# Optimization experiments

Hardware: AMD Instinct MI355X
Metric: run time of the kernel (lower is better)

## Reference

```python
import jax, jax.numpy as jnp
import numpy as np

NUM_CAMS = 4
E = 256          # embed_dim
H_HEADS = 8      # num_heads
DH = E // H_HEADS
CIN = 64
FF = 4 * E
N_LAYERS = 2
EPS = 1e-5


def _layer_norm(x, g, b):
    mu = jnp.mean(x, axis=-1, keepdims=True)
    var = jnp.mean((x - mu) ** 2, axis=-1, keepdims=True)
    return (x - mu) * jax.lax.rsqrt(var + EPS) * g + b


def setup_inputs() -> dict:
    key = jax.random.key(0)
    ks = jax.random.split(key, 20)
    s = 0.02
    inp = {
        "features": jax.random.normal(ks[0], (NUM_CAMS, 2, CIN, 96, 96), jnp.float32),
        # 1x1 input projection conv
        "Wp": jax.random.normal(ks[1], (E, CIN), jnp.float32) * s,
        "bp": jnp.zeros((E,), jnp.float32),
        # per-layer attention params (stacked over 2 layers)
        "Wqkv": jax.random.normal(ks[2], (N_LAYERS, 3 * E, E), jnp.float32) * s,
        "bqkv": jnp.zeros((N_LAYERS, 3 * E), jnp.float32),
        "Wo": jax.random.normal(ks[3], (N_LAYERS, E, E), jnp.float32) * s,
        "bo": jnp.zeros((N_LAYERS, E), jnp.float32),
        # FFN
        "W1": jax.random.normal(ks[4], (N_LAYERS, FF, E), jnp.float32) * s,
        "b1": jnp.zeros((N_LAYERS, FF), jnp.float32),
        "W2": jax.random.normal(ks[5], (N_LAYERS, E, FF), jnp.float32) * s,
        "b2": jnp.zeros((N_LAYERS, E), jnp.float32),
        # LayerNorms
        "g1": jnp.ones((N_LAYERS, E), jnp.float32),
        "be1": jnp.zeros((N_LAYERS, E), jnp.float32),
        "g2": jnp.ones((N_LAYERS, E), jnp.float32),
        "be2": jnp.zeros((N_LAYERS, E), jnp.float32),
        # 1x1 output conv
        "Wout": jax.random.normal(ks[6], (CIN, E), jnp.float32) * s,
        "bout": jnp.zeros((CIN,), jnp.float32),
    }
    return inp


def reference(features, Wp, bp, Wqkv, bqkv, Wo, bo, W1, b1, W2, b2,
              g1, be1, g2, be2, Wout, bout):
    n_cam, B, Cin, Hh, Ww = features.shape
    # 1x1 conv projection + rearrange to per-pixel sequences: [B*H*W, n_cam, E]
    x = jnp.einsum('nbchw,ec->bhwne', features, Wp) + bp
    x = x.reshape(B * Hh * Ww, n_cam, E)

    scale = 1.0 / jnp.sqrt(jnp.float32(DH))
    for i in range(N_LAYERS):
        # self-attention (post-norm encoder layer, dropout=identity in eval)
        qkv = x @ Wqkv[i].T + bqkv[i]                      # [N, S, 3E]
        q, k, v = jnp.split(qkv, 3, axis=-1)
        q = q.reshape(-1, n_cam, H_HEADS, DH)
        k = k.reshape(-1, n_cam, H_HEADS, DH)
        v = v.reshape(-1, n_cam, H_HEADS, DH)
        scores = jnp.einsum('nqhd,nkhd->nhqk', q, k) * scale
        attn = jax.nn.softmax(scores, axis=-1)
        sa = jnp.einsum('nhqk,nkhd->nqhd', attn, v).reshape(-1, n_cam, E)
        sa = sa @ Wo[i].T + bo[i]
        x = _layer_norm(x + sa, g1[i], be1[i])
        # FFN (ReLU activation, default)
        ff = jax.nn.relu(x @ W1[i].T + b1[i]) @ W2[i].T + b2[i]
        x = _layer_norm(x + ff, g2[i], be2[i])

    # mean over cameras, back to [B, C, H, W] via 1x1 output conv
    fused = x.mean(axis=1).reshape(B, Hh, Ww, E)
    out = jnp.einsum('bhwe,ce->bchw', fused, Wout) + bout[None, :, None, None]
    return out
```

## Files before the change

kernel.cpp:

```cpp
#include <hip/hip_runtime.h>
#include <cstdint>
#include <cstddef>


typedef __bf16 bf16;
typedef __bf16 bf16x8 __attribute__((ext_vector_type(8)));
typedef __bf16 bf16x4 __attribute__((ext_vector_type(4)));
typedef float  f32x4  __attribute__((ext_vector_type(4)));

__device__ __forceinline__ void async_copy16(const void* g, void* l)
{
    __builtin_amdgcn_global_load_lds(
        (__attribute__((address_space(1))) void*)g,
        (__attribute__((address_space(3))) void*)l,
        16, 0, 0);
}

__global__ void pack_all_k(const float* __restrict__ s0, const float* __restrict__ s1,
                           const float* __restrict__ s2, const float* __restrict__ s3,
                           const float* __restrict__ s4,
                           bf16* __restrict__ d0, bf16* __restrict__ d1,
                           bf16* __restrict__ d2, bf16* __restrict__ d3,
                           bf16* __restrict__ d4)
{
    const int i = blockIdx.x * 256 + threadIdx.x;
    if (i < 393216)       d0[i] = (bf16)s0[i];
    else if (i < 524288)  d1[i - 393216] = (bf16)s1[i - 393216];
    else if (i < 1048576) d2[i - 524288] = (bf16)s2[i - 524288];
    else if (i < 1572864) d3[i - 1048576] = (bf16)s3[i - 1048576];
    else                  d4[i - 1572864] = (bf16)s4[i - 1572864];
}

__global__ void pack_w2f_k(const float* __restrict__ W2, bf16* __restrict__ W2F)
{
    const int g  = blockIdx.x * 256 + threadIdx.x;
    const int l  = g >> 15;
    const int e  = g & 32767;
    const int nt   = e >> 11;
    const int rem  = e & 2047;
    const int kc   = rem >> 6;
    const int lane = rem & 63;
    const int row  = nt * 16 + (lane & 15);
    const int col  = kc * 32 + (lane >> 4) * 8;
    const float* src = W2 + (size_t)l * 262144;
    bf16x8 v;
#pragma unroll
    for (int q = 0; q < 8; ++q) v[q] = (bf16)src[(size_t)row * 1024 + col + q];
    *(bf16x8*)(W2F + (size_t)l * 262144 + (size_t)e * 8) = v;
}

__global__ __launch_bounds__(256) void feat_pack_k(const float* __restrict__ feat,
                                                   bf16* __restrict__ Xf)
{
    __shared__ float ft[64][68];

    const int tid  = threadIdx.x;
    const int camb = blockIdx.y;
    const int cam  = camb >> 1;
    const int b    = camb & 1;
    const int hw0  = blockIdx.x * 64;

    const float* fb = feat + (size_t)camb * 64 * 9216 + hw0;
#pragma unroll
    for (int rep = 0; rep < 16; ++rep) {
        const int idx = rep * 256 + tid;
        const int c = idx >> 6, p = idx & 63;
        ft[p][c] = fb[(size_t)c * 9216 + p];
    }
    __syncthreads();

    const int pbase = b * 9216 + hw0;
#pragma unroll
    for (int rep = 0; rep < 2; ++rep) {
        const int idx = rep * 256 + tid;
        const int p = idx >> 3, cc = idx & 7;
        const f32x4 a = *(const f32x4*)(&ft[p][cc * 8]);
        const f32x4 c4 = *(const f32x4*)(&ft[p][cc * 8 + 4]);
        bf16x8 v;
#pragma unroll
        for (int i = 0; i < 4; ++i) { v[i] = (bf16)a[i]; v[4 + i] = (bf16)c4[i]; }
        const size_t t = (size_t)(pbase + p) * 4 + cam;
        *(bf16x8*)(Xf + t * 64 + cc * 8) = v;
    }
}

template <bool RELU>
__global__ __launch_bounds__(256, 2) void gemm_bt(
    const bf16* __restrict__ A, const bf16* __restrict__ B,
    const float* __restrict__ bias, bf16* __restrict__ C,
    int N, int K)
{
    __shared__ __align__(16) bf16 As[128 * 64];
    __shared__ __align__(16) bf16 Bs[128 * 64];

    const int tid  = threadIdx.x;
    const int lane = tid & 63;
    const int wv   = tid >> 6;
    const int wm   = wv >> 1;
    const int wn   = wv & 1;
    const int bm   = blockIdx.y * 128;
    const int bn   = blockIdx.x * 128;

    const int r8  = lane >> 3;
    const int p8  = lane & 7;
    const int gch = p8 ^ r8;

    const int quad = lane >> 4;
    const int l16  = lane & 15;

    f32x4 acc[4][4] = {};

    for (int k0 = 0; k0 < K; k0 += 64) {
#pragma unroll
        for (int inst = 0; inst < 4; ++inst) {
            const int row = wv * 32 + inst * 8 + r8;
            const bf16* ga = A + (size_t)(bm + row) * K + (k0 + gch * 8);
            const bf16* gb = B + (size_t)(bn + row) * K + (k0 + gch * 8);
            async_copy16(ga, (char*)As + (wv * 4 + inst) * 1024);
            async_copy16(gb, (char*)Bs + (wv * 4 + inst) * 1024);
        }
        __syncthreads();

#pragma unroll
        for (int kk = 0; kk < 2; ++kk) {
            bf16x8 af[4], bfr[4];
            const int lch = kk * 4 + quad;
#pragma unroll
            for (int i = 0; i < 4; ++i) {
                const int m = wm * 64 + i * 16 + l16;
                af[i] = *(const bf16x8*)((const char*)As + (m * 8 + (lch ^ (m & 7))) * 16);
                const int n = wn * 64 + i * 16 + l16;
                bfr[i] = *(const bf16x8*)((const char*)Bs + (n * 8 + (lch ^ (n & 7))) * 16);
            }
#pragma unroll
            for (int i = 0; i < 4; ++i)
#pragma unroll
                for (int j = 0; j < 4; ++j)
                    acc[i][j] = __builtin_amdgcn_mfma_f32_16x16x32_bf16(
                        af[i], bfr[j], acc[i][j], 0, 0, 0);
        }
        __syncthreads();
    }

#pragma unroll
    for (int j = 0; j < 4; ++j) {
        const int n = bn + wn * 64 + j * 16 + l16;
        const float bv = bias[n];
#pragma unroll
        for (int i = 0; i < 4; ++i) {
            const int mb = bm + wm * 64 + i * 16 + quad * 4;
#pragma unroll
            for (int r = 0; r < 4; ++r) {
                float v = acc[i][j][r] + bv;
                if (RELU) v = fmaxf(v, 0.f);
                C[(size_t)(mb + r) * N + n] = (bf16)v;
            }
        }
    }
}

__global__ __launch_bounds__(256, 2) void gemm_ln_k(
    const bf16* __restrict__ A, const bf16* __restrict__ B,
    const float* __restrict__ bias, const bf16* __restrict__ Xres,
    const float* __restrict__ gam, const float* __restrict__ bet,
    bf16* __restrict__ Xout, int K)
{
    __shared__ __align__(16) bf16 S[24576];
    __shared__ float2 red[128][2];

    const int tid  = threadIdx.x;
    const int lane = tid & 63;
    const int wv   = tid >> 6;
    const int wm   = wv >> 1;
    const int wn   = wv & 1;
    const int bm   = blockIdx.x * 128;
    const int quad = lane >> 4;
    const int l16  = lane & 15;

    f32x4 acc[4][8] = {};

    for (int k0 = 0; k0 < K; k0 += 64) {
#pragma unroll
        for (int s = 0; s < 12; ++s) {
            const int L   = s * 256 + tid;
            const int row = L >> 3;
            const int gch = (L & 7) ^ (row & 7);
            const bf16* g = (row < 128)
                ? A + (size_t)(bm + row) * K + (k0 + gch * 8)
                : B + (size_t)(row - 128) * K + (k0 + gch * 8);
            async_copy16(g, (char*)S + (size_t)L * 16);
        }
        __syncthreads();

#pragma unroll
        for (int kk = 0; kk < 2; ++kk) {
            const int lch = kk * 4 + quad;
            bf16x8 af[4], bfr[8];
#pragma unroll
            for (int i = 0; i < 4; ++i) {
                const int m = wm * 64 + i * 16 + l16;
                af[i] = *(const bf16x8*)((const char*)S + (m * 8 + (lch ^ (m & 7))) * 16);
            }
#pragma unroll
            for (int j = 0; j < 8; ++j) {
                const int n = wn * 128 + j * 16 + l16;
                bfr[j] = *(const bf16x8*)((const char*)S + ((128 + n) * 8 + (lch ^ (n & 7))) * 16);
            }
#pragma unroll
            for (int i = 0; i < 4; ++i)
#pragma unroll
                for (int j = 0; j < 8; ++j)
                    acc[i][j] = __builtin_amdgcn_mfma_f32_16x16x32_bf16(
                        af[i], bfr[j], acc[i][j], 0, 0, 0);
        }
        __syncthreads();
    }

    float bv[8], gv[8], bev[8];
#pragma unroll
    for (int j = 0; j < 8; ++j) {
        const int n = wn * 128 + j * 16 + l16;
        bv[j] = bias[n]; gv[j] = gam[n]; bev[j] = bet[n];
    }

#pragma unroll
    for (int i = 0; i < 4; ++i) {
#pragma unroll
        for (int r = 0; r < 4; ++r) {
            const int rl  = wm * 64 + i * 16 + quad * 4 + r;
            const size_t row = (size_t)(bm + rl);
            float s1 = 0.f, s2 = 0.f;
#pragma unroll
            for (int j = 0; j < 8; ++j) {
                const int n = wn * 128 + j * 16 + l16;
                const float v = acc[i][j][r] + bv[j] + (float)Xres[row * 256 + n];
                acc[i][j][r] = v;
                s1 += v; s2 += v * v;
            }
#pragma unroll
            for (int off = 1; off < 16; off <<= 1) {
                s1 += __shfl_xor(s1, off, 64);
                s2 += __shfl_xor(s2, off, 64);
            }
            if (l16 == 0) red[rl][wn] = make_float2(s1, s2);
        }
    }
    __syncthreads();

#pragma unroll
    for (int i = 0; i < 4; ++i) {
#pragma unroll
        for (int r = 0; r < 4; ++r) {
            const int rl = wm * 64 + i * 16 + quad * 4 + r;
            const float2 p0 = red[rl][0], p1 = red[rl][1];
            const float mu  = (p0.x + p1.x) * (1.f / 256.f);
            const float ex2 = (p0.y + p1.y) * (1.f / 256.f);
            const float rstd = rsqrtf(fmaxf(ex2 - mu * mu, 0.f) + 1e-5f);
            const size_t row = (size_t)(bm + rl);
#pragma unroll
            for (int j = 0; j < 8; ++j) {
                const int n = wn * 128 + j * 16 + l16;
                Xout[row * 256 + n] = (bf16)((acc[i][j][r] - mu) * rstd * gv[j] + bev[j]);
            }
        }
    }
}

__device__ __forceinline__ void ffn_stage_w1(int st, const bf16* __restrict__ W1,
                                             char* stg, int tid)
{
    char* buf = stg + (size_t)(st & 1) * 16384;
    const int hc = st >> 2;
    const int q  = st & 3;
#pragma unroll
    for (int it = 0; it < 4; ++it) {
        const int L = it * 256 + tid;
        const int row = L >> 3, psl = L & 7;
        const int c = psl ^ (row & 7);
        async_copy16(W1 + (size_t)(hc * 128 + row) * 256 + q * 64 + c * 8,
                     buf + (size_t)L * 16);
    }
}

__global__ __launch_bounds__(256, 2) void ffn_fused_k(
    const bf16* __restrict__ X,
    const bf16* __restrict__ W1, const float* __restrict__ b1,
    const bf16* __restrict__ W2f, const float* __restrict__ b2,
    const float* __restrict__ gam, const float* __restrict__ bet,
    bf16* __restrict__ Xout)
{
    __shared__ __align__(16) char smem[81920];
    bf16* Xs = (bf16*)smem;
    bf16* Ts = (bf16*)(smem + 32768);
    float2 (*red)[2] = (float2 (*)[2])(void*)(smem + 32768);
    char* stg = smem + 49152;

    const int tid  = threadIdx.x;
    const int lane = tid & 63;
    const int wv   = tid >> 6;
    const int wm   = wv >> 1;
    const int wn   = wv & 1;
    const int quad = lane >> 4;
    const int l16  = lane & 15;
    const int bm   = blockIdx.x * 64;

#pragma unroll
    for (int it = 0; it < 8; ++it) {
        const int L = it * 256 + tid;
        const int row = L >> 5, slot = L & 31;
        const int gch = (slot & 24) | ((slot ^ row) & 7);
        async_copy16(X + (size_t)(bm + row) * 256 + gch * 8,
                     (char*)Xs + (size_t)L * 16);
    }
    ffn_stage_w1(0, W1, stg, tid);
    __syncthreads();

    f32x4 acc2[2][8] = {};

#pragma unroll 1
    for (int hc = 0; hc < 8; ++hc) {
        f32x4 accA[2][4] = {};

#pragma unroll
        for (int q = 0; q < 4; ++q) {
            const int st = hc * 4 + q;
            if (st + 1 < 32) ffn_stage_w1(st + 1, W1, stg, tid);
            const char* cur = stg + (size_t)(st & 1) * 16384;
#pragma unroll
            for (int kk = 0; kk < 2; ++kk) {
                const int ch = kk * 4 + quad;
                const int gc = q * 8 + ch;
                bf16x8 af[2], bfr[4];
#pragma unroll
                for (int i = 0; i < 2; ++i) {
                    const int m  = wm * 32 + i * 16 + l16;
                    const int sl = (gc & 24) | ((gc ^ m) & 7);
                    af[i] = *(const bf16x8*)((const char*)Xs + (m * 32 + sl) * 16);
                }
#pragma unroll
                for (int j = 0; j < 4; ++j) {
                    const int n  = wn * 64 + j * 16 + l16;
                    const int sl = ch ^ (n & 7);
                    bfr[j] = *(const bf16x8*)(cur + (n * 8 + sl) * 16);
                }
#pragma unroll
                for (int i = 0; i < 2; ++i)
#pragma unroll
                    for (int j = 0; j < 4; ++j)
                        accA[i][j] = __builtin_amdgcn_mfma_f32_16x16x32_bf16(
                            af[i], bfr[j], accA[i][j], 0, 0, 0);
            }
            if (q == 3) {
#pragma unroll
                for (int j = 0; j < 4; ++j) {
                    const int h  = wn * 64 + j * 16 + l16;
                    const float bb = b1[hc * 128 + h];
                    const int g  = h >> 3;
#pragma unroll
                    for (int i = 0; i < 2; ++i)
#pragma unroll
                        for (int r = 0; r < 4; ++r) {
                            const int m  = wm * 32 + i * 16 + quad * 4 + r;
                            const int sl = (g & 8) | ((g ^ m) & 7);
                            const float v = fmaxf(accA[i][j][r] + bb, 0.f);
                            *((bf16*)((char*)Ts + (m * 16 + sl) * 16 + (h & 7) * 2)) = (bf16)v;
                        }
                }
            }
            __syncthreads();
        }

#pragma unroll 2
        for (int kc = 0; kc < 4; ++kc) {
            const int tc = kc * 4 + quad;
            bf16x8 af[2], bfr[8];
#pragma unroll
            for (int i = 0; i < 2; ++i) {
                const int m  = wm * 32 + i * 16 + l16;
                const int sl = (tc & 8) | ((tc ^ m) & 7);
                af[i] = *(const bf16x8*)((const char*)Ts + (m * 16 + sl) * 16);
            }
            const int kcg = hc * 4 + kc;
#pragma unroll
            for (int j = 0; j < 8; ++j) {
                const int nt = wn * 8 + j;
                bfr[j] = *(const bf16x8*)(W2f + ((size_t)(nt * 32 + kcg) * 64 + lane) * 8);
            }
#pragma unroll
            for (int i = 0; i < 2; ++i)
#pragma unroll
                for (int j = 0; j < 8; ++j)
                    acc2[i][j] = __builtin_amdgcn_mfma_f32_16x16x32_bf16(
                        af[i], bfr[j], acc2[i][j], 0, 0, 0);
        }
    }

    __syncthreads();

    float bv[8], gv[8], bev[8];
#pragma unroll
    for (int j = 0; j < 8; ++j) {
        const int n = wn * 128 + j * 16 + l16;
        bv[j] = b2[n]; gv[j] = gam[n]; bev[j] = bet[n];
    }

#pragma unroll
    for (int i = 0; i < 2; ++i) {
#pragma unroll
        for (int r = 0; r < 4; ++r) {
            const int rl = wm * 32 + i * 16 + quad * 4 + r;
            float s1 = 0.f, s2 = 0.f;
#pragma unroll
            for (int j = 0; j < 8; ++j) {
                const int n  = wn * 128 + j * 16 + l16;
                const int gc = n >> 3;
                const int sl = (gc & 24) | ((gc ^ rl) & 7);
                const float xr = (float)*((const bf16*)((const char*)Xs +
                                   (rl * 32 + sl) * 16 + (n & 7) * 2));
                const float v = acc2[i][j][r] + bv[j] + xr;
                acc2[i][j][r] = v;
                s1 += v; s2 += v * v;
            }
#pragma unroll
            for (int off = 1; off < 16; off <<= 1) {
                s1 += __shfl_xor(s1, off, 64);
                s2 += __shfl_xor(s2, off, 64);
            }
            if (l16 == 0) red[rl][wn] = make_float2(s1, s2);
        }
    }
    __syncthreads();

#pragma unroll
    for (int i = 0; i < 2; ++i) {
#pragma unroll
        for (int r = 0; r < 4; ++r) {
            const int rl = wm * 32 + i * 16 + quad * 4 + r;
            const float2 p0 = red[rl][0], p1 = red[rl][1];
            const float mu  = (p0.x + p1.x) * (1.f / 256.f);
            const float ex2 = (p0.y + p1.y) * (1.f / 256.f);
            const float rstd = rsqrtf(fmaxf(ex2 - mu * mu, 0.f) + 1e-5f);
            const size_t row = (size_t)(bm + rl);
#pragma unroll
            for (int j = 0; j < 8; ++j) {
                const int n = wn * 128 + j * 16 + l16;
                Xout[row * 256 + n] = (bf16)((acc2[i][j][r] - mu) * rstd * gv[j] + bev[j]);
            }
        }
    }
}

__global__ __launch_bounds__(256) void attention_k(const bf16* __restrict__ QKV,
                                                   bf16* __restrict__ SA)
{
    __shared__ float qf[4][4][768];
    __shared__ float sc[4][8][4][4];

    const int tid  = threadIdx.x;
    const int wv   = tid >> 6;
    const int lane = tid & 63;
    const int s    = blockIdx.x * 4 + wv;

    const bf16* base = QKV + (size_t)s * 4 * 768;
#pragma unroll
    for (int it = 0; it < 6; ++it) {
        const int idx = it * 64 + lane;
        const bf16x8 v = *(const bf16x8*)(base + idx * 8);
        const int tok = idx / 96;
        const int e   = (idx % 96) * 8;
        f32x4 f0, f1;
#pragma unroll
        for (int i = 0; i < 4; ++i) { f0[i] = (float)v[i]; f1[i] = (float)v[4 + i]; }
        *(f32x4*)(&qf[wv][tok][e])     = f0;
        *(f32x4*)(&qf[wv][tok][e + 4]) = f1;
    }
    __syncthreads();

#pragma unroll
    for (int rep = 0; rep < 2; ++rep) {
        const int t = rep * 64 + lane;
        const int h = t >> 4, i = (t >> 2) & 3, j = t & 3;
        const float* q = &qf[wv][i][h * 32];
        const float* k = &qf[wv][j][256 + h * 32];
        float a = 0.f;
#pragma unroll
        for (int dd = 0; dd < 32; ++dd) {
            const int d = (dd + lane) & 31;
            a += q[d] * k[d];
        }
        sc[wv][h][i][j] = a * 0.17677669529663687f;
    }
    __syncthreads();

    if (lane < 32) {
        const int h = lane >> 2, i = lane & 3;
        float s0 = sc[wv][h][i][0], s1 = sc[wv][h][i][1];
        float s2 = sc[wv][h][i][2], s3 = sc[wv][h][i][3];
        float m = fmaxf(fmaxf(s0, s1), fmaxf(s2, s3));
        float e0 = expf(s0 - m), e1 = expf(s1 - m);
        float e2 = expf(s2 - m), e3 = expf(s3 - m);
        float inv = 1.f / (e0 + e1 + e2 + e3);
        sc[wv][h][i][0] = e0 * inv;
        sc[wv][h][i][1] = e1 * inv;
        sc[wv][h][i][2] = e2 * inv;
        sc[wv][h][i][3] = e3 * inv;
    }
    __syncthreads();

    const int h = lane >> 3;
#pragma unroll
    for (int i = 0; i < 4; ++i) {
        f32x4 a = {0.f, 0.f, 0.f, 0.f};
#pragma unroll
        for (int j = 0; j < 4; ++j) {
            const float p = sc[wv][h][i][j];
            const f32x4 v = *(const f32x4*)(&qf[wv][j][512 + lane * 4]);
#pragma unroll
            for (int q = 0; q < 4; ++q) a[q] += p * v[q];
        }
        bf16x4 o;
#pragma unroll
        for (int q = 0; q < 4; ++q) o[q] = (bf16)a[q];
        *(bf16x4*)(SA + (size_t)(s * 4 + i) * 256 + lane * 4) = o;
    }
}

__global__ __launch_bounds__(256) void out_proj_k(const bf16* __restrict__ X,
                                                  const float* __restrict__ Wout,
                                                  const float* __restrict__ bout,
                                                  float* __restrict__ out)
{
    __shared__ float fused[16][260];
    const int tid = threadIdx.x;
    const int p0  = blockIdx.x * 16;

#pragma unroll
    for (int it = 0; it < 16; ++it) {
        const int idx = it * 256 + tid;
        const int pix = idx >> 8, e = idx & 255;
        const size_t base = (size_t)(p0 + pix) * 1024 + e;
        const float s = (float)X[base] + (float)X[base + 256] +
                        (float)X[base + 512] + (float)X[base + 768];
        fused[pix][e] = s * 0.25f;
    }
    __syncthreads();

    const int pix = tid & 15;
    const int c0  = tid >> 4;
    const int p   = p0 + pix;
    const int b   = p / 9216;
    const int hw  = p % 9216;
#pragma unroll
    for (int it = 0; it < 4; ++it) {
        const int c = it * 16 + c0;
        const float* w = Wout + c * 256;
        float acc = bout[c];
#pragma unroll 8
        for (int e = 0; e < 256; ++e) acc += fused[pix][e] * w[e];
        out[((size_t)b * 64 + c) * 9216 + hw] = acc;
    }
}

extern "C" void kernel_launch(void* const* d_in, const int* in_sizes, int n_in,
                              void* d_out, int out_size, void* d_ws, size_t ws_size,
                              hipStream_t stream)
{
    const float* features = (const float*)d_in[0];
    const float* Wp   = (const float*)d_in[1];
    const float* bp   = (const float*)d_in[2];
    const float* Wqkv = (const float*)d_in[3];
    const float* bqkv = (const float*)d_in[4];
    const float* Wo   = (const float*)d_in[5];
    const float* bo   = (const float*)d_in[6];
    const float* W1   = (const float*)d_in[7];
    const float* b1   = (const float*)d_in[8];
    const float* W2   = (const float*)d_in[9];
    const float* b2   = (const float*)d_in[10];
    const float* g1   = (const float*)d_in[11];
    const float* be1  = (const float*)d_in[12];
    const float* g2   = (const float*)d_in[13];
    const float* be2  = (const float*)d_in[14];
    const float* Wout = (const float*)d_in[15];
    const float* bout = (const float*)d_in[16];
    float* out = (float*)d_out;

    char* ws = (char*)d_ws;
    bf16* X   = (bf16*)(ws);
    bf16* QKV = (bf16*)(ws + 37748736ull);
    bf16* SAb = (bf16*)(ws + 150994944ull);
    bf16* Xf  = (bf16*)(ws + 188743680ull);
    bf16* WpB = (bf16*)(ws + 198180864ull);
    bf16* W2F = (bf16*)(ws + 198213632ull);
    bf16* Wb  = (bf16*)(ws + 226492416ull);

    bf16* WqkvB = Wb;
    bf16* WoB   = Wb + 393216;
    bf16* W1B   = Wb + 524288;

    pack_all_k<<<6208, 256, 0, stream>>>(Wqkv, Wo, W1, W2, Wp,
                                         WqkvB, WoB, W1B, Wb + 1048576, WpB);
    pack_w2f_k<<<256, 256, 0, stream>>>(W2, W2F);

    feat_pack_k<<<dim3(144, 8), 256, 0, stream>>>(features, Xf);
    gemm_bt<false><<<dim3(2, 576), 256, 0, stream>>>(Xf, WpB, bp, X, 256, 64);

    for (int l = 0; l < 2; ++l) {
        gemm_bt<false><<<dim3(6, 576), 256, 0, stream>>>(
            X, WqkvB + l * 196608, bqkv + l * 768, QKV, 768, 256);
        attention_k<<<4608, 256, 0, stream>>>(QKV, SAb);
        gemm_ln_k<<<576, 256, 0, stream>>>(
            SAb, WoB + l * 65536, bo + l * 256, X,
            g1 + l * 256, be1 + l * 256, X, 256);
        ffn_fused_k<<<1152, 256, 0, stream>>>(
            X, W1B + l * 262144, b1 + l * 1024,
            W2F + l * 262144, b2 + l * 256,
            g2 + l * 256, be2 + l * 256, X);
    }

    out_proj_k<<<1152, 256, 0, stream>>>(X, Wout, bout, out);
}
```

Baseline: 661.8 us.

## Pre-swizzle W1 and Wqkv into MFMA fragment layout, read B directly from global

Weights for the QKV projection and the FFN's first matmul are repacked once into the MFMA B-fragment order. The kernels then load B operands straight from global (L2-cached) memory instead of staging them in LDS through double buffers. A new dedicated QKV GEMM keeps the whole 128x256 A tile in LDS. This removes LDS staging traffic and most barriers in the FFN and shrinks its LDS footprint, at the cost of global-latency-bound B loads that are no longer prefetched.

```diff
diff --git a/kernel.cpp b/kernel.cpp
--- a/kernel.cpp
+++ b/kernel.cpp
@@ -16,37 +16,40 @@
         16, 0, 0);
 }
 
-__global__ void pack_all_k(const float* __restrict__ s0, const float* __restrict__ s1,
-                           const float* __restrict__ s2, const float* __restrict__ s3,
-                           const float* __restrict__ s4,
-                           bf16* __restrict__ d0, bf16* __restrict__ d1,
-                           bf16* __restrict__ d2, bf16* __restrict__ d3,
-                           bf16* __restrict__ d4)
+__global__ void pack_all_k(const float* __restrict__ Wo, const float* __restrict__ Wp,
+                           bf16* __restrict__ WoB, bf16* __restrict__ WpB)
 {
     const int i = blockIdx.x * 256 + threadIdx.x;
-    if (i < 393216)       d0[i] = (bf16)s0[i];
-    else if (i < 524288)  d1[i - 393216] = (bf16)s1[i - 393216];
-    else if (i < 1048576) d2[i - 524288] = (bf16)s2[i - 524288];
-    else if (i < 1572864) d3[i - 1048576] = (bf16)s3[i - 1048576];
-    else                  d4[i - 1572864] = (bf16)s4[i - 1572864];
-}
-
-__global__ void pack_w2f_k(const float* __restrict__ W2, bf16* __restrict__ W2F)
-{
-    const int g  = blockIdx.x * 256 + threadIdx.x;
-    const int l  = g >> 15;
-    const int e  = g & 32767;
-    const int nt   = e >> 11;
-    const int rem  = e & 2047;
+    if (i < 131072)      WoB[i] = (bf16)Wo[i];
+    else if (i < 147456) WpB[i - 131072] = (bf16)Wp[i - 131072];
+}
+
+__global__ void pack_frag_k(const float* __restrict__ W1, const float* __restrict__ W2,
+                            const float* __restrict__ Wqkv,
+                            bf16* __restrict__ W1F, bf16* __restrict__ W2F,
+                            bf16* __restrict__ WqkvF)
+{
+    const int g = blockIdx.x * 256 + threadIdx.x;
+    const float* src; bf16* dst; int K, e;
+    if (g < 65536)       { const int l = g >> 15; e = g & 32767; K = 256;
+                           src = W1 + (size_t)l * 262144;  dst = W1F + (size_t)l * 262144; }
+    else if (g < 131072) { const int r = g - 65536; const int l = r >> 15; e = r & 32767; K = 1024;
+                           src = W2 + (size_t)l * 262144;  dst = W2F + (size_t)l * 262144; }
+    else if (g < 180224) { const int r = g - 131072; const int l = r / 24576; e = r % 24576; K = 256;
+                           src = Wqkv + (size_t)l * 196608; dst = WqkvF + (size_t)l * 196608; }
+    else return;
+
+    const int perNT = (K >> 5) << 6;
+    const int nt   = e / perNT;
+    const int rem  = e % perNT;
     const int kc   = rem >> 6;
     const int lane = rem & 63;
     const int row  = nt * 16 + (lane & 15);
     const int col  = kc * 32 + (lane >> 4) * 8;
-    const float* src = W2 + (size_t)l * 262144;
     bf16x8 v;
 #pragma unroll
-    for (int q = 0; q < 8; ++q) v[q] = (bf16)src[(size_t)row * 1024 + col + q];
-    *(bf16x8*)(W2F + (size_t)l * 262144 + (size_t)e * 8) = v;
+    for (int q = 0; q < 8; ++q) v[q] = (bf16)src[(size_t)row * K + col + q];
+    *(bf16x8*)(dst + (size_t)e * 8) = v;
 }
 
 __global__ __launch_bounds__(256) void feat_pack_k(const float* __restrict__ feat,
@@ -155,6 +158,71 @@
                 if (RELU) v = fmaxf(v, 0.f);
                 C[(size_t)(mb + r) * N + n] = (bf16)v;
             }
+        }
+    }
+}
+
+__global__ __launch_bounds__(256, 2) void gemm_qkv_k(
+    const bf16* __restrict__ A, const bf16* __restrict__ Bf,
+    const float* __restrict__ bias, bf16* __restrict__ C)
+{
+    __shared__ __align__(16) char As[65536];
+
+    const int tid  = threadIdx.x;
+    const int lane = tid & 63;
+    const int wv   = tid >> 6;
+    const int wm   = wv >> 1;
+    const int wn   = wv & 1;
+    const int bm   = blockIdx.y * 128;
+    const int bn   = blockIdx.x * 128;
+    const int nt0  = blockIdx.x * 8;
+    const int quad = lane >> 4;
+    const int l16  = lane & 15;
+
+#pragma unroll
+    for (int it = 0; it < 16; ++it) {
+        const int L = it * 256 + tid;
+        const int row = L >> 5, s = L & 31;
+        const int c = (s & 24) | ((s ^ row) & 7);
+        async_copy16(A + (size_t)(bm + row) * 256 + c * 8, As + (size_t)L * 16);
+    }
+    __syncthreads();
+
+    f32x4 acc[4][4] = {};
+
+#pragma unroll 2
+    for (int kk = 0; kk < 8; ++kk) {
+        bf16x8 af[4], bfr[4];
+        const int gc = kk * 4 + quad;
+#pragma unroll
+        for (int i = 0; i < 4; ++i) {
+            const int m  = wm * 64 + i * 16 + l16;
+            const int sl = (gc & 24) | ((gc ^ m) & 7);
+            af[i] = *(const bf16x8*)(As + (size_t)(m * 32 + sl) * 16);
+        }
+#pragma unroll
+        for (int j = 0; j < 4; ++j) {
+            const int nt = nt0 + wn * 4 + j;
+            bfr[j] = *(const bf16x8*)(Bf + ((size_t)(nt * 8 + kk) * 64 + lane) * 8);
+        }
+#pragma unroll
+        for (int i = 0; i < 4; ++i)
+#pragma unroll
+            for (int j = 0; j < 4; ++j)
+                acc[i][j] = __builtin_amdgcn_mfma_f32_16x16x32_bf16(
+                    af[i], bfr[j], acc[i][j], 0, 0, 0);
+    }
+
+#pragma unroll
+    for (int j = 0; j < 4; ++j) {
+        const int n = bn + wn * 64 + j * 16 + l16;
+        const float bv = bias[n];
+#pragma unroll
+        for (int i = 0; i < 4; ++i) {
+            const int mb = bm + wm * 64 + i * 16 + quad * 4;
+#pragma unroll
+            for (int r = 0; r < 4; ++r)
+                C[(size_t)(mb + r) * 768 + n] = (bf16)(acc[i][j][r] + bv);
         }
     }
 }
@@ -266,34 +334,17 @@
     }
 }
 
-__device__ __forceinline__ void ffn_stage_w1(int st, const bf16* __restrict__ W1,
-                                             char* stg, int tid)
-{
-    char* buf = stg + (size_t)(st & 1) * 16384;
-    const int hc = st >> 2;
-    const int q  = st & 3;
-#pragma unroll
-    for (int it = 0; it < 4; ++it) {
-        const int L = it * 256 + tid;
-        const int row = L >> 3, psl = L & 7;
-        const int c = psl ^ (row & 7);
-        async_copy16(W1 + (size_t)(hc * 128 + row) * 256 + q * 64 + c * 8,
-                     buf + (size_t)L * 16);
-    }
-}
-
 __global__ __launch_bounds__(256, 2) void ffn_fused_k(
     const bf16* __restrict__ X,
-    const bf16* __restrict__ W1, const float* __restrict__ b1,
+    const bf16* __restrict__ W1f, const float* __restrict__ b1,
     const bf16* __restrict__ W2f, const float* __restrict__ b2,
     const float* __restrict__ gam, const float* __restrict__ bet,
     bf16* __restrict__ Xout)
 {
-    __shared__ __align__(16) char smem[81920];
+    __shared__ __align__(16) char smem[49152];
     bf16* Xs = (bf16*)smem;
     bf16* Ts = (bf16*)(smem + 32768);
     float2 (*red)[2] = (float2 (*)[2])(void*)(smem + 32768);
-    char* stg = smem + 49152;
 
     const int tid  = threadIdx.x;
     const int lane = tid & 63;
@@ -312,7 +363,6 @@
         async_copy16(X + (size_t)(bm + row) * 256 + gch * 8,
                      (char*)Xs + (size_t)L * 16);
     }
-    ffn_stage_w1(0, W1, stg, tid);
     __syncthreads();
 
     f32x4 acc2[2][8] = {};
@@ -321,54 +371,47 @@
     for (int hc = 0; hc < 8; ++hc) {
         f32x4 accA[2][4] = {};
 
-#pragma unroll
-        for (int q = 0; q < 4; ++q) {
-            const int st = hc * 4 + q;
-            if (st + 1 < 32) ffn_stage_w1(st + 1, W1, stg, tid);
-            const char* cur = stg + (size_t)(st & 1) * 16384;
-#pragma unroll
-            for (int kk = 0; kk < 2; ++kk) {
-                const int ch = kk * 4 + quad;
-                const int gc = q * 8 + ch;
-                bf16x8 af[2], bfr[4];
-#pragma unroll
-                for (int i = 0; i < 2; ++i) {
-                    const int m  = wm * 32 + i * 16 + l16;
-                    const int sl = (gc & 24) | ((gc ^ m) & 7);
-                    af[i] = *(const bf16x8*)((const char*)Xs + (m * 32 + sl) * 16);
+#pragma unroll 2
+        for (int kk = 0; kk < 8; ++kk) {
+            bf16x8 af[2], bfr[4];
+            const int gc = kk * 4 + quad;
+#pragma unroll
+            for (int i = 0; i < 2; ++i) {
+                const int m  = wm * 32 + i * 16 + l16;
+                const int sl = (gc & 24) | ((gc ^ m) & 7);
+                af[i] = *(const bf16x8*)((const char*)Xs + (m * 32 + sl) * 16);
+            }
+#pragma unroll
+            for (int j = 0; j < 4; ++j) {
+                const int nt = hc * 8 + wn * 4 + j;
+                bfr[j] = *(const bf16x8*)(W1f + ((size_t)(nt * 8 + kk) * 64 + lane) * 8);
+            }
+#pragma unroll
+            for (int i = 0; i < 2; ++i)
+#pragma unroll
+                for (int j = 0; j < 4; ++j)
+                    accA[i][j] = __builtin_amdgcn_mfma_f32_16x16x32_bf16(
+                        af[i], bfr[j], accA[i][j], 0, 0, 0);
+        }
+
+        __syncthreads();
+
+#pragma unroll
+        for (int j = 0; j < 4; ++j) {
+            const int h  = wn * 64 + j * 16 + l16;
+            const float bb = b1[hc * 128 + h];
+            const int g  = h >> 3;
+#pragma unroll
+            for (int i = 0; i < 2; ++i)
+#pragma unroll
+                for (int r = 0; r < 4; ++r) {
+                    const int m  = wm * 32 + i * 16 + quad * 4 + r;
+                    const int sl = (g & 8) | ((g ^ m) & 7);
+                    const float v = fmaxf(accA[i][j][r] + bb, 0.f);
+                    *((bf16*)((char*)Ts + (m * 16 + sl) * 16 + (h & 7) * 2)) = (bf16)v;
                 }
-#pragma unroll
-                for (int j = 0; j < 4; ++j) {
-                    const int n  = wn * 64 + j * 16 + l16;
-                    const int sl = ch ^ (n & 7);
-                    bfr[j] = *(const bf16x8*)(cur + (n * 8 + sl) * 16);
-                }
-#pragma unroll
-                for (int i = 0; i < 2; ++i)
-#pragma unroll
-                    for (int j = 0; j < 4; ++j)
-                        accA[i][j] = __builtin_amdgcn_mfma_f32_16x16x32_bf16(
-                            af[i], bfr[j], accA[i][j], 0, 0, 0);
-            }
-            if (q == 3) {
-#pragma unroll
-                for (int j = 0; j < 4; ++j) {
-                    const int h  = wn * 64 + j * 16 + l16;
-                    const float bb = b1[hc * 128 + h];
-                    const int g  = h >> 3;
-#pragma unroll
-                    for (int i = 0; i < 2; ++i)
-#pragma unroll
-                        for (int r = 0; r < 4; ++r) {
-                            const int m  = wm * 32 + i * 16 + quad * 4 + r;
-                            const int sl = (g & 8) | ((g ^ m) & 7);
-                            const float v = fmaxf(accA[i][j][r] + bb, 0.f);
-                            *((bf16*)((char*)Ts + (m * 16 + sl) * 16 + (h & 7) * 2)) = (bf16)v;
-                        }
-                }
-            }
-            __syncthreads();
-        }
+        }
+        __syncthreads();
 
 #pragma unroll 2
         for (int kc = 0; kc < 4; ++kc) {
@@ -585,34 +628,31 @@
     float* out = (float*)d_out;
 
     char* ws = (char*)d_ws;
-    bf16* X   = (bf16*)(ws);
-    bf16* QKV = (bf16*)(ws + 37748736ull);
-    bf16* SAb = (bf16*)(ws + 150994944ull);
-    bf16* Xf  = (bf16*)(ws + 188743680ull);
-    bf16* WpB = (bf16*)(ws + 198180864ull);
-    bf16* W2F = (bf16*)(ws + 198213632ull);
-    bf16* Wb  = (bf16*)(ws + 226492416ull);
-
-    bf16* WqkvB = Wb;
-    bf16* WoB   = Wb + 393216;
-    bf16* W1B   = Wb + 524288;
-
-    pack_all_k<<<6208, 256, 0, stream>>>(Wqkv, Wo, W1, W2, Wp,
-                                         WqkvB, WoB, W1B, Wb + 1048576, WpB);
-    pack_w2f_k<<<256, 256, 0, stream>>>(W2, W2F);
+    bf16* X     = (bf16*)(ws);
+    bf16* QKV   = (bf16*)(ws + 37748736ull);
+    bf16* SAb   = (bf16*)(ws + 150994944ull);
+    bf16* Xf    = (bf16*)(ws + 188743680ull);
+    bf16* WpB   = (bf16*)(ws + 198180864ull);
+    bf16* W2F   = (bf16*)(ws + 198213632ull);
+    bf16* W1F   = (bf16*)(ws + 199262208ull);
+    bf16* WqkvF = (bf16*)(ws + 200310784ull);
+    bf16* WoB   = (bf16*)(ws + 226492416ull);
+
+    pack_all_k<<<576, 256, 0, stream>>>(Wo, Wp, WoB, WpB);
+    pack_frag_k<<<704, 256, 0, stream>>>(W1, W2, Wqkv, W1F, W2F, WqkvF);
 
     feat_pack_k<<<dim3(144, 8), 256, 0, stream>>>(features, Xf);
     gemm_bt<false><<<dim3(2, 576), 256, 0, stream>>>(Xf, WpB, bp, X, 256, 64);
 
     for (int l = 0; l < 2; ++l) {
-        gemm_bt<false><<<dim3(6, 576), 256, 0, stream>>>(
-            X, WqkvB + l * 196608, bqkv + l * 768, QKV, 768, 256);
+        gemm_qkv_k<<<dim3(6, 576), 256, 0, stream>>>(
+            X, WqkvF + l * 196608, bqkv + l * 768, QKV);
         attention_k<<<4608, 256, 0, stream>>>(QKV, SAb);
         gemm_ln_k<<<576, 256, 0, stream>>>(
             SAb, WoB + l * 65536, bo + l * 256, X,
             g1 + l * 256, be1 + l * 256, X, 256);
         ffn_fused_k<<<1152, 256, 0, stream>>>(
-            X, W1B + l * 262144, b1 + l * 1024,
+            X, W1F + l * 262144, b1 + l * 1024,
             W2F + l * 262144, b2 + l * 256,
             g2 + l * 256, be2 + l * 256, X);
     }
```

Result: slower. 787.6 us (+19.0%).
